# Performance work log

Hardware: AMD Instinct MI355X
Metric: run time of the kernel (lower is better)

## Reference

```python
import jax, jax.numpy as jnp
import numpy as np


def setup_inputs() -> dict:
    key = jax.random.key(0)
    k1, k2, k3 = jax.random.split(key, 3)
    B, T, I, H, D = 32, 1024, 1024, 16, 64
    x = jax.random.normal(k1, (B, T, I), dtype=jnp.float32)
    kv_kernel = jax.random.normal(k2, (I, H, D, 2), dtype=jnp.float32) * (1.0 / np.sqrt(I))
    q_kernel = jax.random.normal(k3, (H, D), dtype=jnp.float32) * (1.0 / np.sqrt(D))
    return {"x": x, "kv_kernel": kv_kernel, "q_kernel": q_kernel}


def _attention_rnn(x, kv_kernel, q_kernel):
    # x: [B,T,I]; kv_kernel: [I,H,D,2]; q_kernel: [H,D]
    B, T, _ = x.shape
    H, D = q_kernel.shape
    # Projection + silu activation, done once for all timesteps (same math as per-step einsum)
    kv = jnp.einsum('bti,ihdk->bthdk', x, kv_kernel)
    kv = jax.nn.silu(kv)
    k = kv[..., 0]  # [B,T,H,D]
    v = kv[..., 1]  # [B,T,H,D]
    # Per-step attention score s_t = <q_h, k_th>
    s = jnp.einsum('hd,bthd->bth', q_kernel, k)  # [B,T,H]

    # Keras RNN zero-initialized states: num [B,H,D], den [B,H], max [B,H]
    init = (
        jnp.zeros((B, H, D), x.dtype),
        jnp.zeros((B, H), x.dtype),
        jnp.zeros((B, H), x.dtype),
    )

    def step(carry, inp):
        num, den, pmax = carry
        s_t, v_t = inp  # [B,H], [B,H,D]
        cmax = jnp.maximum(pmax, s_t)
        exp_max_diff = jnp.exp(pmax - cmax)
        sm = jnp.exp(s_t - cmax)
        den_n = sm + den * exp_max_diff
        num_n = v_t * sm[..., None] + num * exp_max_diff[..., None]
        h = num_n / den_n[..., None]          # [B,H,D]
        o = jnp.sum(h, axis=-2)               # concat_heads=False -> sum over heads: [B,D]
        return (num_n, den_n, cmax), o

    # scan over time (leading axis)
    _, outs = jax.lax.scan(step, init, (jnp.swapaxes(s, 0, 1), jnp.swapaxes(v, 0, 1)))
    return jnp.swapaxes(outs, 0, 1)  # [B,T,D]


def reference(x, kv_kernel, q_kernel):
    return _attention_rnn(x, kv_kernel, q_kernel)
```

## Files before the change

### kernel.cpp

```cpp
#include <hip/hip_runtime.h>
#include <hip/hip_bf16.h>

#define B_ 32
#define T_ 1024
#define H_ 16
#define D_ 64
#define M_ (B_*T_)
#define N_ (H_*D_*2)
#define K_ 1024
#define CHUNKS 16
#define CLEN (T_/CHUNKS)

typedef __bf16 bf16x8 __attribute__((ext_vector_type(8)));
typedef float  f32x4  __attribute__((ext_vector_type(4)));

__device__ __forceinline__ float bf2f(unsigned short u){
  union{ float f; unsigned int i; } c; c.i = ((unsigned int)u) << 16; return c.f;
}
__device__ __forceinline__ unsigned short f2bf(float f){
  union{ float f; unsigned int i; } c; c.f = f;
  unsigned int r = (c.i + 0x7FFFu + ((c.i >> 16) & 1u)) >> 16;
  return (unsigned short)r;
}
__device__ __forceinline__ float silu(float x){ return x / (1.0f + __expf(-x)); }

__device__ __forceinline__ void gload16(const void* g, void* l){
  __builtin_amdgcn_global_load_lds(
      (const __attribute__((address_space(1))) void*)g,
      (__attribute__((address_space(3))) void*)l, 16, 0, 0);
}

#define BAR()   __builtin_amdgcn_s_barrier()
#define LGKM0() asm volatile("s_waitcnt lgkmcnt(0)" ::: "memory")
#define VM4()   asm volatile("s_waitcnt vmcnt(4)" ::: "memory")

__global__ __launch_bounds__(256) void cvt_x(const float* __restrict__ x,
                                             unsigned short* __restrict__ xb, int n){
  int i = (blockIdx.x * 256 + threadIdx.x) * 4;
  int stride = gridDim.x * 256 * 4;
  for(; i < n; i += stride){
    float4 v = *(const float4*)(x + i);
    ushort4 o;
    o.x = f2bf(v.x); o.y = f2bf(v.y); o.z = f2bf(v.z); o.w = f2bf(v.w);
    *(ushort4*)(xb + i) = o;
  }
}

__global__ __launch_bounds__(256) void cvt_w(const float* __restrict__ w,
                                             unsigned short* __restrict__ wt){
  __shared__ unsigned short tile[64][65];
  int kt = blockIdx.x * 64, nt = blockIdx.y * 64;
  int t = threadIdx.x, tn = t & 63, tk4 = t >> 6;
  #pragma unroll
  for(int r = 0; r < 16; ++r){
    int kl = r * 4 + tk4;
    tile[tn][kl] = f2bf(w[(kt + kl) * N_ + nt + tn]);
  }
  __syncthreads();
  #pragma unroll
  for(int r = 0; r < 16; ++r){
    int nl = r * 4 + tk4;
    int n  = nt + nl;
    int np = (n & ~127) | ((n & 1) << 6) | ((n >> 1) & 63);
    wt[(size_t)np * K_ + kt + tn] = tile[nl][tn];
  }
}

__global__ __launch_bounds__(512, 2) void gemm8(
    const unsigned short* __restrict__ xb,
    const unsigned short* __restrict__ wt,
    const float*  __restrict__ q,
    unsigned short* __restrict__ vout,
    float* __restrict__ s)
{
  __shared__ __align__(16) char lds[131072];

  const int t = threadIdx.x, lane = t & 63, wid = t >> 6;
  const int wr = wid >> 2, wc = wid & 3;
  const int l15 = lane & 15, l4 = lane >> 4;

  const int id  = blockIdx.y * gridDim.x + blockIdx.x;
  const int swz = (id & 7) * 128 + (id >> 3);
  const int bx = swz & 127, by = swz >> 7;
  const int brow = bx * 256, bcol = by * 256;

  f32x4 acc[8][4] = {};
  bf16x8 af[8], b0[4], b1[4];

  const int swl   = l15 & 7;
  const int aoff0 = l15 * 128 + (((0 + l4) ^ swl) << 4);
  const int aoff1 = l15 * 128 + (((4 + l4) ^ swl) << 4);

  auto stage = [&](int buf, int op, int half, const unsigned short* src,
                   int rowbase, int kt){
    char* base = lds + buf * 65536 + op * 32768 + half * 16384;
    #pragma unroll
    for(int L = 0; L < 2; ++L){
      int idx = L * 512 + t;
      int r = idx >> 3, ss = idx & 7;
      gload16(src + (size_t)(rowbase + half * 128 + r) * K_
                  + kt * 64 + ((ss ^ (r & 7)) << 3),
              base + idx * 16);
    }
  };
  auto rdA = [&](int buf, int miBase){
    const char* base = lds + buf * 65536 + wr * 16384;
    #pragma unroll
    for(int m = 0; m < 4; ++m){
      af[m*2+0] = *(const bf16x8*)(base + (miBase + m) * 2048 + aoff0);
      af[m*2+1] = *(const bf16x8*)(base + (miBase + m) * 2048 + aoff1);
    }
  };
  auto rdB = [&](int buf, int niBase, bf16x8 (&dst)[4]){
    const char* base = lds + buf * 65536 + 32768 + (wc >> 1) * 16384 + (wc & 1) * 8192;
    #pragma unroll
    for(int n = 0; n < 2; ++n){
      dst[n*2+0] = *(const bf16x8*)(base + (niBase + n) * 2048 + aoff0);
      dst[n*2+1] = *(const bf16x8*)(base + (niBase + n) * 2048 + aoff1);
    }
  };
  auto mmaq = [&](int miBase, bf16x8 (&bb)[4], int niBase){
    __builtin_amdgcn_s_setprio(1);
    #pragma unroll
    for(int m = 0; m < 4; ++m)
      #pragma unroll
      for(int n = 0; n < 2; ++n)
        #pragma unroll
        for(int k = 0; k < 2; ++k)
          acc[miBase+m][niBase+n] = __builtin_amdgcn_mfma_f32_16x16x32_bf16(
              af[m*2+k], bb[n*2+k], acc[miBase+m][niBase+n], 0, 0, 0);
    __builtin_amdgcn_s_setprio(0);
  };

  stage(0,0,0, xb, brow, 0); stage(0,0,1, xb, brow, 0);
  stage(0,1,0, wt, bcol, 0); stage(0,1,1, wt, bcol, 0);
  stage(1,1,0, wt, bcol, 1); stage(1,1,1, wt, bcol, 1);
  VM4(); BAR();

  for(int i = 0; i < 8; ++i){
    const int t1 = 2*i + 1;
    const int t2 = (2*i + 2) & 15;
    const int t3 = (2*i + 3) & 15;
    rdA(0,0); rdB(0,0,b0); stage(1,0,0, xb, brow, t1);
    BAR(); LGKM0(); mmaq(0,b0,0); BAR();
    rdB(0,2,b1); stage(1,0,1, xb, brow, t1);
    BAR(); LGKM0(); mmaq(0,b1,2); BAR();
    rdA(0,4); stage(0,1,0, wt, bcol, t2);
    BAR(); LGKM0(); mmaq(4,b1,2); BAR();
    stage(0,1,1, wt, bcol, t2); VM4();
    BAR(); mmaq(4,b0,0); BAR();
    rdA(1,0); rdB(1,0,b0); stage(0,0,0, xb, brow, t2);
    BAR(); LGKM0(); mmaq(0,b0,0); BAR();
    rdB(1,2,b1); stage(0,0,1, xb, brow, t2);
    BAR(); LGKM0(); mmaq(0,b1,2); BAR();
    rdA(1,4); stage(1,1,0, wt, bcol, t3);
    BAR(); LGKM0(); mmaq(4,b1,2); BAR();
    stage(1,1,1, wt, bcol, t3); VM4();
    BAR(); mmaq(4,b0,0); BAR();
  }

  __syncthreads();

  const int hh = by * 2 + (wc >> 1);
  if(wc & 1){
    #pragma unroll
    for(int mi = 0; mi < 8; ++mi)
      #pragma unroll
      for(int r = 0; r < 4; ++r){
        const int gm = brow + wr*128 + mi*16 + l4*4 + r;
        const int bb = gm >> 10, tt = gm & (T_-1);
        unsigned short* vrow = vout + (((size_t)bb*H_ + hh)*T_ + tt)*D_;
        #pragma unroll
        for(int ni = 0; ni < 4; ++ni)
          vrow[ni*16 + l15] = f2bf(silu(acc[mi][ni][r]));
      }
  } else {
    float qv[4];
    #pragma unroll
    for(int ni = 0; ni < 4; ++ni) qv[ni] = q[hh*D_ + ni*16 + l15];
    #pragma unroll
    for(int mi = 0; mi < 8; ++mi)
      #pragma unroll
      for(int r = 0; r < 4; ++r){
        float sc = 0.f;
        #pragma unroll
        for(int ni = 0; ni < 4; ++ni) sc += qv[ni] * silu(acc[mi][ni][r]);
        sc += __shfl_xor(sc, 1); sc += __shfl_xor(sc, 2);
        sc += __shfl_xor(sc, 4); sc += __shfl_xor(sc, 8);
        if(l15 == 0){
          const int gm = brow + wr*128 + mi*16 + l4*4 + r;
          s[(size_t)gm * H_ + hh] = sc;
        }
      }
  }
}

__global__ __launch_bounds__(64) void scan1(
    const unsigned short* __restrict__ v, const float* __restrict__ s,
    float* __restrict__ snum, float* __restrict__ sden, float* __restrict__ smax)
{
  const int blk = blockIdx.x;
  const int c = blk & (CHUNKS-1), bh = blk / CHUNKS;
  const int b = bh >> 4, h = bh & 15, lane = threadIdx.x;
  float m = -3.0e38f, den = 0.f, num = 0.f;
  const unsigned short* vb = v + (((size_t)b*H_ + h)*T_ + c*CLEN)*D_;
  const float* sb = s + ((size_t)b*T_ + c*CLEN)*H_ + h;
  for(int tt = 0; tt < CLEN; ++tt){
    float st = sb[tt*H_];
    float vt = bf2f(vb[tt*D_ + lane]);
    float cm = fmaxf(m, st);
    float e  = __expf(m - cm);
    float p  = __expf(st - cm);
    den = den * e + p;
    num = num * e + p * vt;
    m = cm;
  }
  snum[blk*64 + lane] = num;
  if(lane == 0){ sden[blk] = den; smax[blk] = m; }
}

__global__ __launch_bounds__(256) void scan2h(
    const unsigned short* __restrict__ v, const float* __restrict__ s,
    const float* __restrict__ snum, const float* __restrict__ sden,
    const float* __restrict__ smax, float* __restrict__ out)
{
  __shared__ float sst[CLEN*H_];
  __shared__ float oacc[4][CLEN][D_];
  const int blk = blockIdx.x;
  const int c = blk & (CHUNKS-1), b = blk >> 4;
  const int t = threadIdx.x, lane = t & 63, w = t >> 6;

  const float* sbase = s + ((size_t)b*T_ + c*CLEN) * H_;
  for(int i = t; i < CLEN*H_; i += 256) sst[i] = sbase[i];
  __syncthreads();

  const int h0 = w * 4;
  float num[4], den[4], m[4];
  #pragma unroll
  for(int j = 0; j < 4; ++j){ num[j] = 0.f; den[j] = 0.f; m[j] = -3.0e38f; }

  for(int cc = 0; cc < c; ++cc){
    #pragma unroll
    for(int j = 0; j < 4; ++j){
      int sb = (b*H_ + h0 + j)*CHUNKS + cc;
      float m2 = smax[sb], d2 = sden[sb], n2 = snum[sb*64 + lane];
      float cm = fmaxf(m[j], m2);
      float e1 = __expf(m[j]-cm), e2 = __expf(m2-cm);
      den[j] = den[j]*e1 + d2*e2;
      num[j] = num[j]*e1 + n2*e2;
      m[j] = cm;
    }
  }

  const unsigned short* vb = v + (((size_t)b*H_ + h0)*T_ + c*CLEN)*D_;
  for(int tt = 0; tt < CLEN; ++tt){
    float o = 0.f;
    #pragma unroll
    for(int j = 0; j < 4; ++j){
      float st = sst[tt*H_ + h0 + j];
      float vt = bf2f(vb[(size_t)j*T_*D_ + tt*D_ + lane]);
      float cm = fmaxf(m[j], st);
      float e = __expf(m[j]-cm), p = __expf(st-cm);
      den[j] = den[j]*e + p;
      num[j] = num[j]*e + p*vt;
      m[j] = cm;
      o += num[j] / den[j];
    }
    oacc[w][tt][lane] = o;
  }
  __syncthreads();

  {
    int tt = t >> 2, db = (t & 3) * 16;
    float* ob = out + ((size_t)b*T_ + c*CLEN + tt) * D_ + db;
    #pragma unroll
    for(int qd = 0; qd < 4; ++qd){
      f32x4 a0 = *(const f32x4*)&oacc[0][tt][db + qd*4];
      f32x4 a1 = *(const f32x4*)&oacc[1][tt][db + qd*4];
      f32x4 a2 = *(const f32x4*)&oacc[2][tt][db + qd*4];
      f32x4 a3 = *(const f32x4*)&oacc[3][tt][db + qd*4];
      f32x4 r = (a0 + a1) + (a2 + a3);
      *(f32x4*)(ob + qd*4) = r;
    }
  }
}

extern "C" void kernel_launch(void* const* d_in, const int* in_sizes, int n_in,
                              void* d_out, int out_size, void* d_ws, size_t ws_size,
                              hipStream_t stream){
  (void)in_sizes; (void)n_in; (void)out_size; (void)ws_size;
  const float* x = (const float*)d_in[0];
  const float* w = (const float*)d_in[1];
  const float* q = (const float*)d_in[2];
  float* out = (float*)d_out;
  char* ws = (char*)d_ws;

  unsigned short* wt   = (unsigned short*)(ws);
  unsigned short* xb   = (unsigned short*)(ws + (4u  << 20));
  unsigned short* vbuf = (unsigned short*)(ws + (68u << 20));
  float* s    = (float*)(ws + (132u << 20));
  float* snum = (float*)(ws + (134u << 20));
  float* sden = (float*)(ws + (136u << 20));
  float* smax = (float*)(ws + (136u << 20) + (1u << 15));

  cvt_x<<<2048, 256, 0, stream>>>(x, xb, M_ * K_);
  cvt_w<<<dim3(K_/64, N_/64), 256, 0, stream>>>(w, wt);
  gemm8<<<dim3(M_/256, N_/256), 512, 0, stream>>>(xb, wt, q, vbuf, s);
  scan1<<<B_*H_*CHUNKS, 64, 0, stream>>>(vbuf, s, snum, sden, smax);
  scan2h<<<B_*CHUNKS, 256, 0, stream>>>(vbuf, s, snum, sden, smax, out);
}
```

Baseline: 253.0 us.

## Rebalance chunked scan, peel GEMM tail, widen x conversion, pad output tile

Doubles the number of time chunks in the two-pass scan. The first scan pass is rebuilt so one 256-thread block handles all heads of a (batch, chunk) pair, with scores staged in shared memory, mirroring the second pass. The GEMM main loop is peeled so the last iteration no longer issues wrapped-around prefetches, and a full vmcnt wait is used at the end. The x fp32-to-bf16 conversion now processes 8 elements per thread with 16-byte stores, and the scan2 output staging buffer is padded to reduce LDS bank conflicts. The chunk-summary buffers are moved into the x-conversion region, which is safe only because the GEMM has finished reading it before the scans run. More chunks also means more serial combine work in the second pass.

```diff
diff --git a/kernel.cpp b/kernel.cpp
--- a/kernel.cpp
+++ b/kernel.cpp
@@ -8,11 +8,12 @@
 #define M_ (B_*T_)
 #define N_ (H_*D_*2)
 #define K_ 1024
-#define CHUNKS 16
+#define CHUNKS 32
 #define CLEN (T_/CHUNKS)
 
 typedef __bf16 bf16x8 __attribute__((ext_vector_type(8)));
 typedef float  f32x4  __attribute__((ext_vector_type(4)));
+typedef unsigned short u16x8 __attribute__((ext_vector_type(8)));
 
 __device__ __forceinline__ float bf2f(unsigned short u){
   union{ float f; unsigned int i; } c; c.i = ((unsigned int)u) << 16; return c.f;
@@ -33,16 +34,19 @@
 #define BAR()   __builtin_amdgcn_s_barrier()
 #define LGKM0() asm volatile("s_waitcnt lgkmcnt(0)" ::: "memory")
 #define VM4()   asm volatile("s_waitcnt vmcnt(4)" ::: "memory")
+#define VM0()   asm volatile("s_waitcnt vmcnt(0)" ::: "memory")
 
 __global__ __launch_bounds__(256) void cvt_x(const float* __restrict__ x,
                                              unsigned short* __restrict__ xb, int n){
-  int i = (blockIdx.x * 256 + threadIdx.x) * 4;
-  int stride = gridDim.x * 256 * 4;
+  int i = (blockIdx.x * 256 + threadIdx.x) * 8;
+  int stride = gridDim.x * 256 * 8;
   for(; i < n; i += stride){
-    float4 v = *(const float4*)(x + i);
-    ushort4 o;
-    o.x = f2bf(v.x); o.y = f2bf(v.y); o.z = f2bf(v.z); o.w = f2bf(v.w);
-    *(ushort4*)(xb + i) = o;
+    float4 v0 = *(const float4*)(x + i);
+    float4 v1 = *(const float4*)(x + i + 4);
+    u16x8 o;
+    o[0]=f2bf(v0.x); o[1]=f2bf(v0.y); o[2]=f2bf(v0.z); o[3]=f2bf(v0.w);
+    o[4]=f2bf(v1.x); o[5]=f2bf(v1.y); o[6]=f2bf(v1.z); o[7]=f2bf(v1.w);
+    *(u16x8*)(xb + i) = o;
   }
 }
 
@@ -137,10 +141,10 @@
   stage(1,1,0, wt, bcol, 1); stage(1,1,1, wt, bcol, 1);
   VM4(); BAR();
 
-  for(int i = 0; i < 8; ++i){
+  for(int i = 0; i < 7; ++i){
     const int t1 = 2*i + 1;
-    const int t2 = (2*i + 2) & 15;
-    const int t3 = (2*i + 3) & 15;
+    const int t2 = 2*i + 2;
+    const int t3 = 2*i + 3;
     rdA(0,0); rdB(0,0,b0); stage(1,0,0, xb, brow, t1);
     BAR(); LGKM0(); mmaq(0,b0,0); BAR();
     rdB(0,2,b1); stage(1,0,1, xb, brow, t1);
@@ -158,8 +162,21 @@
     stage(1,1,1, wt, bcol, t3); VM4();
     BAR(); mmaq(4,b0,0); BAR();
   }
-
-  __syncthreads();
+  rdA(0,0); rdB(0,0,b0); stage(1,0,0, xb, brow, 15);
+  BAR(); LGKM0(); mmaq(0,b0,0); BAR();
+  rdB(0,2,b1); stage(1,0,1, xb, brow, 15);
+  BAR(); LGKM0(); mmaq(0,b1,2); BAR();
+  rdA(0,4);
+  BAR(); LGKM0(); mmaq(4,b1,2); BAR();
+  VM0();
+  BAR(); mmaq(4,b0,0); BAR();
+  rdA(1,0); rdB(1,0,b0);
+  BAR(); LGKM0(); mmaq(0,b0,0); BAR();
+  rdB(1,2,b1);
+  BAR(); LGKM0(); mmaq(0,b1,2); BAR();
+  rdA(1,4);
+  BAR(); LGKM0(); mmaq(4,b1,2); BAR();
+  mmaq(4,b0,0);
 
   const int hh = by * 2 + (wc >> 1);
   if(wc & 1){
@@ -195,28 +212,43 @@
   }
 }
 
-__global__ __launch_bounds__(64) void scan1(
+__global__ __launch_bounds__(256) void scan1(
     const unsigned short* __restrict__ v, const float* __restrict__ s,
     float* __restrict__ snum, float* __restrict__ sden, float* __restrict__ smax)
 {
+  __shared__ float sst[CLEN*H_];
   const int blk = blockIdx.x;
-  const int c = blk & (CHUNKS-1), bh = blk / CHUNKS;
-  const int b = bh >> 4, h = bh & 15, lane = threadIdx.x;
-  float m = -3.0e38f, den = 0.f, num = 0.f;
-  const unsigned short* vb = v + (((size_t)b*H_ + h)*T_ + c*CLEN)*D_;
-  const float* sb = s + ((size_t)b*T_ + c*CLEN)*H_ + h;
+  const int c = blk & (CHUNKS-1), b = blk >> 5;
+  const int t = threadIdx.x, lane = t & 63, w = t >> 6, h0 = w * 4;
+
+  const float* sbase = s + ((size_t)b*T_ + c*CLEN) * H_;
+  for(int i = t; i < CLEN*H_; i += 256) sst[i] = sbase[i];
+  __syncthreads();
+
+  float m[4], den[4], num[4];
+  #pragma unroll
+  for(int j = 0; j < 4; ++j){ m[j] = -3.0e38f; den[j] = 0.f; num[j] = 0.f; }
+
+  const unsigned short* vb = v + (((size_t)b*H_ + h0)*T_ + c*CLEN)*D_;
   for(int tt = 0; tt < CLEN; ++tt){
-    float st = sb[tt*H_];
-    float vt = bf2f(vb[tt*D_ + lane]);
-    float cm = fmaxf(m, st);
-    float e  = __expf(m - cm);
-    float p  = __expf(st - cm);
-    den = den * e + p;
-    num = num * e + p * vt;
-    m = cm;
-  }
-  snum[blk*64 + lane] = num;
-  if(lane == 0){ sden[blk] = den; smax[blk] = m; }
+    #pragma unroll
+    for(int j = 0; j < 4; ++j){
+      float st = sst[tt*H_ + h0 + j];
+      float vt = bf2f(vb[(size_t)j*T_*D_ + tt*D_ + lane]);
+      float cm = fmaxf(m[j], st);
+      float e  = __expf(m[j] - cm);
+      float p  = __expf(st - cm);
+      den[j] = den[j]*e + p;
+      num[j] = num[j]*e + p*vt;
+      m[j] = cm;
+    }
+  }
+  #pragma unroll
+  for(int j = 0; j < 4; ++j){
+    int sb = (b*H_ + h0 + j)*CHUNKS + c;
+    snum[(size_t)sb*64 + lane] = num[j];
+    if(lane == 0){ sden[sb] = den[j]; smax[sb] = m[j]; }
+  }
 }
 
 __global__ __launch_bounds__(256) void scan2h(
@@ -225,16 +257,15 @@
     const float* __restrict__ smax, float* __restrict__ out)
 {
   __shared__ float sst[CLEN*H_];
-  __shared__ float oacc[4][CLEN][D_];
+  __shared__ float oacc[4][CLEN][76];
   const int blk = blockIdx.x;
-  const int c = blk & (CHUNKS-1), b = blk >> 4;
-  const int t = threadIdx.x, lane = t & 63, w = t >> 6;
+  const int c = blk & (CHUNKS-1), b = blk >> 5;
+  const int t = threadIdx.x, lane = t & 63, w = t >> 6, h0 = w * 4;
 
   const float* sbase = s + ((size_t)b*T_ + c*CLEN) * H_;
   for(int i = t; i < CLEN*H_; i += 256) sst[i] = sbase[i];
   __syncthreads();
 
-  const int h0 = w * 4;
   float num[4], den[4], m[4];
   #pragma unroll
   for(int j = 0; j < 4; ++j){ num[j] = 0.f; den[j] = 0.f; m[j] = -3.0e38f; }
@@ -243,7 +274,7 @@
     #pragma unroll
     for(int j = 0; j < 4; ++j){
       int sb = (b*H_ + h0 + j)*CHUNKS + cc;
-      float m2 = smax[sb], d2 = sden[sb], n2 = snum[sb*64 + lane];
+      float m2 = smax[sb], d2 = sden[sb], n2 = snum[(size_t)sb*64 + lane];
       float cm = fmaxf(m[j], m2);
       float e1 = __expf(m[j]-cm), e2 = __expf(m2-cm);
       den[j] = den[j]*e1 + d2*e2;
@@ -271,10 +302,10 @@
   __syncthreads();
 
   {
-    int tt = t >> 2, db = (t & 3) * 16;
+    int tt = t >> 3, db = (t & 7) * 8;
     float* ob = out + ((size_t)b*T_ + c*CLEN + tt) * D_ + db;
     #pragma unroll
-    for(int qd = 0; qd < 4; ++qd){
+    for(int qd = 0; qd < 2; ++qd){
       f32x4 a0 = *(const f32x4*)&oacc[0][tt][db + qd*4];
       f32x4 a1 = *(const f32x4*)&oacc[1][tt][db + qd*4];
       f32x4 a2 = *(const f32x4*)&oacc[2][tt][db + qd*4];
@@ -299,13 +330,13 @@
   unsigned short* xb   = (unsigned short*)(ws + (4u  << 20));
   unsigned short* vbuf = (unsigned short*)(ws + (68u << 20));
   float* s    = (float*)(ws + (132u << 20));
-  float* snum = (float*)(ws + (134u << 20));
-  float* sden = (float*)(ws + (136u << 20));
-  float* smax = (float*)(ws + (136u << 20) + (1u << 15));
+  float* snum = (float*)(ws + (8u  << 20));
+  float* sden = (float*)(ws + (12u << 20));
+  float* smax = (float*)(ws + (12u << 20) + (1u << 16));
 
   cvt_x<<<2048, 256, 0, stream>>>(x, xb, M_ * K_);
   cvt_w<<<dim3(K_/64, N_/64), 256, 0, stream>>>(w, wt);
   gemm8<<<dim3(M_/256, N_/256), 512, 0, stream>>>(xb, wt, q, vbuf, s);
-  scan1<<<B_*H_*CHUNKS, 64, 0, stream>>>(vbuf, s, snum, sden, smax);
+  scan1<<<B_*CHUNKS, 256, 0, stream>>>(vbuf, s, snum, sden, smax);
   scan2h<<<B_*CHUNKS, 256, 0, stream>>>(vbuf, s, snum, sden, smax, out);
 }
```

New measurement: 259.6 us. 2.6% more time.
